# Kernel tuning notes

Hardware: AMD Instinct MI355X
Metric: run time of the kernel (lower is better)

Reference implementation:

```python
import jax, jax.numpy as jnp
import numpy as np
from jax import lax

B, C, H, W = 16, 128, 96, 96
G, S = 4, 2            # DySample groups, scale
CO = 2 * G * S * S     # offset channels = 32
COUT = 64              # EUCB2 out_channels
BN_EPS = 1e-5


def conv2d(x, w, pad=0, dil=1, groups=1):
    return lax.conv_general_dilated(
        x, w, (1, 1), [(pad, pad), (pad, pad)],
        rhs_dilation=(dil, dil), feature_group_count=groups,
        dimension_numbers=('NCHW', 'OIHW', 'NCHW'))


def init_pos():
    # torch: arange((-s+1)/2,(s-1)/2+1)/s ; meshgrid ij ; stack ; transpose(1,2) ; repeat(1,G,1)
    h = (jnp.arange(S, dtype=jnp.float32) - (S - 1) / 2) / S
    gy, gx = jnp.meshgrid(h, h, indexing='ij')
    m = jnp.stack([gy, gx])                 # [2,S,S]
    m = jnp.swapaxes(m, 1, 2)               # transpose(1,2)
    m = jnp.tile(m, (1, G, 1))              # [2, S*G, S]
    return m.reshape(1, -1, 1, 1)           # [1, 2*G*S^2, 1, 1]


def grid_sample_border(x, grid):
    # x: [N,Cg,H,W], grid: [N,Ho,Wo,2] (x,y in [-1,1]), align_corners=False, border pad
    N, Cg, Hi, Wi = x.shape
    Ho, Wo = grid.shape[1], grid.shape[2]
    ix = jnp.clip(((grid[..., 0] + 1.0) * Wi - 1.0) * 0.5, 0.0, Wi - 1.0)
    iy = jnp.clip(((grid[..., 1] + 1.0) * Hi - 1.0) * 0.5, 0.0, Hi - 1.0)
    x0f = jnp.floor(ix); y0f = jnp.floor(iy)
    wx = (ix - x0f)[:, None]                # [N,1,Ho,Wo]
    wy = (iy - y0f)[:, None]
    x0 = jnp.clip(x0f.astype(jnp.int32), 0, Wi - 1)
    x1 = jnp.clip(x0 + 1, 0, Wi - 1)
    y0 = jnp.clip(y0f.astype(jnp.int32), 0, Hi - 1)
    y1 = jnp.clip(y0 + 1, 0, Hi - 1)
    flat = x.reshape(N, Cg, Hi * Wi)

    def gather(yi, xi):
        idx = (yi * Wi + xi).reshape(N, -1)
        return jax.vmap(lambda f, i: f[:, i])(flat, idx).reshape(N, Cg, Ho, Wo)

    v00 = gather(y0, x0); v01 = gather(y0, x1)
    v10 = gather(y1, x0); v11 = gather(y1, x1)
    return (v00 * (1 - wx) * (1 - wy) + v01 * wx * (1 - wy)
            + v10 * (1 - wx) * wy + v11 * wx * wy)


def setup_inputs() -> dict:
    key = jax.random.key(0)
    ks = jax.random.split(key, 11)
    inp = {
        'x': jax.random.normal(ks[0], (B, C, H, W), jnp.float32),
        'Wo1': jax.random.normal(ks[1], (CO, C, 1, 1), jnp.float32) * 0.001,
        'bo1': jnp.zeros((CO,), jnp.float32),
        'Wo2': jax.random.normal(ks[2], (CO, CO, 3, 3), jnp.float32) * 0.001,
        'Wdw': jax.random.normal(ks[3], (C, 1, 3, 3), jnp.float32) * 0.3,
        'bn_gamma': jax.random.uniform(ks[4], (C,), jnp.float32) * 0.5 + 0.75,
        'bn_beta': jax.random.normal(ks[5], (C,), jnp.float32) * 0.1,
        'bn_mean': jax.random.normal(ks[6], (C,), jnp.float32) * 0.1,
        'bn_var': jax.random.uniform(ks[7], (C,), jnp.float32) * 0.5 + 0.5,
        'Wpw': jax.random.normal(ks[8], (COUT, C, 1, 1), jnp.float32) / np.sqrt(C),
        'bpw': jax.random.normal(ks[9], (COUT,), jnp.float32) * 0.01,
    }
    return inp


def reference(x, Wo1, bo1, Wo2, Wdw, bn_gamma, bn_beta, bn_mean, bn_var, Wpw, bpw):
    # ---- offset branch: 1x1 conv (+bias) -> 3x3 dilated(2) conv (no bias) ----
    off = conv2d(x, Wo1) + bo1[:, None, None]
    off = conv2d(off, Wo2, pad=2, dil=2)
    offset = off / G + init_pos()                    # [B, 2*G*S^2, H, W]

    # ---- DySample.sample ----
    Bc, _, Hc, Wc = offset.shape
    offset = offset.reshape(Bc, 2, G * S * S, Hc, Wc)
    ar_h = jnp.arange(Hc, dtype=jnp.float32)
    ar_w = jnp.arange(Wc, dtype=jnp.float32)
    ch = ar_h + jnp.sin(jnp.pi * (ar_h + 1.0) / Hc)
    cw = ar_w + jnp.sin(jnp.pi * (ar_w + 1.0) / Wc)
    # channel 0 -> x coord (varies with w), channel 1 -> y coord (varies with h)
    base = jnp.stack([jnp.broadcast_to(cw[None, :], (Hc, Wc)),
                      jnp.broadcast_to(ch[:, None], (Hc, Wc))])   # [2,H,W]
    norm = jnp.array([Wc, Hc], jnp.float32).reshape(1, 2, 1, 1, 1)
    coords = 2.0 * (base[None, :, None] + offset) / norm - 1.0     # [B,2,G*S^2,H,W]

    # pixel_shuffle(scale=S) on [B, 2*G*S^2, H, W]
    coords = coords.reshape(Bc, 2, G, S, S, Hc, Wc)
    coords = coords.transpose(0, 1, 2, 5, 3, 6, 4)                 # [B,2,G,H,S,W,S]
    coords = coords.reshape(Bc, 2, G, S * Hc, S * Wc)
    grid = coords.transpose(0, 2, 3, 4, 1).reshape(Bc * G, S * Hc, S * Wc, 2)

    up = grid_sample_border(x.reshape(Bc * G, C // G, Hc, Wc), grid)
    up = up.reshape(Bc, C, S * Hc, S * Wc)                         # [B,C,2H,2W]

    # ---- EUCB2: depthwise conv -> BN -> ReLU -> channel_shuffle(C) -> 1x1 conv ----
    y = conv2d(up, Wdw, pad=1, groups=C)
    y = (y - bn_mean[:, None, None]) * (bn_gamma[:, None, None]
        * lax.rsqrt(bn_var + BN_EPS)[:, None, None]) + bn_beta[:, None, None]
    y = jax.nn.relu(y)
    # channel_shuffle with groups == num_channels => channels_per_group = 1 => identity
    out = conv2d(y, Wpw) + bpw[:, None, None]
    return out
```

## Files before the change

### kernel.cpp

```cpp
#include <hip/hip_runtime.h>
#include <math.h>

typedef _Float16 f16x8 __attribute__((ext_vector_type(8)));
typedef _Float16 f16x2 __attribute__((ext_vector_type(2)));
typedef float f32x4 __attribute__((ext_vector_type(4)));

namespace {
constexpr int B_ = 16, C_ = 128, H_ = 96, W_ = 96;
constexpr int HW_ = H_ * W_;
constexpr int G_ = 4, S_ = 2;
constexpr int CO_ = 32;
constexpr int COUT_ = 64;
constexpr int HO_ = 192, WO_ = 192;
constexpr int HWO_ = HO_ * WO_;
constexpr int CPG_ = C_ / G_;
constexpr int TH_ = 8, TW_ = 32;
constexpr int HALO_H = TH_ + 2, HALO_W = TW_ + 2;
constexpr int NPOS = HALO_H * HALO_W;
constexpr int NITEM = NPOS * 4;
constexpr int TILES = (WO_ / TW_) * (HO_ / TH_);
constexpr int BPI = HW_ / 256;
constexpr int XPB = HW_ / 64;

constexpr size_t WS_XT     = 0;
constexpr size_t WS_OFF1T  = 9437184;
constexpr size_t WS_SREC   = 11796480;
constexpr size_t WS_WPWH   = 16515072;
constexpr size_t WS_WO1H   = 16519168;
constexpr size_t WS_WO2H   = 16521216;
constexpr size_t WS_WDWSH  = 16525824;
constexpr size_t WS_BIAS2H = 16526400;
constexpr size_t WS_Y      = 16526464;
constexpr size_t IMG_YF16  = (size_t)G_ * 4 * HWO_ * 8;
constexpr size_t Y_FULL_F  = (size_t)B_ * IMG_YF16 / 2;
constexpr size_t NEED_FULL = (WS_Y + Y_FULL_F) * 4;
constexpr size_t NEED_MID  = (WS_Y + Y_FULL_F / 2) * 4;

constexpr int PREP_N = 8192 + 4096 + 9216 + 1152 + 128;
}

__device__ __forceinline__ f16x8 splat8(_Float16 s) {
  return (f16x8){s, s, s, s, s, s, s, s};
}
__device__ __forceinline__ unsigned short h2u(_Float16 h) {
  union { unsigned short u; _Float16 h; } c; c.h = h; return c.u;
}
__device__ __forceinline__ _Float16 u2h(unsigned short u) {
  union { unsigned short u; _Float16 h; } c; c.u = u; return c.h;
}

__global__ __launch_bounds__(256) void k_prep(
    const float* __restrict__ Wpw, const float* __restrict__ Wo1,
    const float* __restrict__ Wo2, const float* __restrict__ Wdw,
    const float* __restrict__ bn_gamma, const float* __restrict__ bn_beta,
    const float* __restrict__ bn_mean, const float* __restrict__ bn_var,
    _Float16* __restrict__ wpwH, _Float16* __restrict__ wo1H,
    _Float16* __restrict__ wo2H, _Float16* __restrict__ wdwSh,
    _Float16* __restrict__ bias2h) {
  int i = blockIdx.x * 256 + threadIdx.x;
  if (i < 8192) {
    wpwH[i] = (_Float16)Wpw[i];
  } else if (i < 8192 + 4096) {
    int j = i - 8192;
    wo1H[j] = (_Float16)Wo1[j];
  } else if (i < 8192 + 4096 + 9216) {
    int j = i - 8192 - 4096;
    int o = j / 288, r = j % 288;
    int tap = r / 32, ci = r % 32;
    wo2H[j] = (_Float16)Wo2[o * 288 + ci * 9 + tap];
  } else if (i < 8192 + 4096 + 9216 + 1152) {
    int j = i - 8192 - 4096 - 9216;
    int c = j / 9, t = j % 9;
    float sc = bn_gamma[c] * rsqrtf(bn_var[c] + 1e-5f);
    wdwSh[t * C_ + c] = (_Float16)(Wdw[j] * sc);
  } else if (i < PREP_N) {
    int c = i - (8192 + 4096 + 9216 + 1152);
    float sc = bn_gamma[c] * rsqrtf(bn_var[c] + 1e-5f);
    bias2h[c] = (_Float16)(bn_beta[c] - bn_mean[c] * sc);
  }
}

__global__ __launch_bounds__(256, 4) void k_xpose(const float* __restrict__ x,
                                                  _Float16* __restrict__ xT) {
  __shared__ float t[64][130];
  int bid = blockIdx.x;
  int swz = (bid & 7) * (B_ * XPB / 8) + (bid >> 3);
  int b = swz / XPB, px0 = (swz % XPB) * 64;
  int tid = threadIdx.x;
  int lane = tid & 63, wv = tid >> 6;
  const float* xb = x + (size_t)b * C_ * HW_ + px0 + lane;
  for (int c = wv; c < C_; c += 4) t[lane][c] = xb[(size_t)c * HW_];
  __syncthreads();
  _Float16* ob = xT + ((size_t)b * HW_ + px0) * C_;
#pragma unroll
  for (int k = 0; k < 4; ++k) {
    int cid = tid + 256 * k;
    int px = cid >> 4, part = cid & 15;
    f16x8 v;
#pragma unroll
    for (int j = 0; j < 8; ++j) v[j] = (_Float16)t[px][part * 8 + j];
    *(f16x8*)&ob[(size_t)px * C_ + part * 8] = v;
  }
}

__global__ __launch_bounds__(256, 4) void k_off1m(
    const _Float16* __restrict__ xT, const _Float16* __restrict__ wo1H,
    const float* __restrict__ bo1, _Float16* __restrict__ off1t) {
  __shared__ float clds[32][257];
  int bid = blockIdx.x;
  int swz = (bid & 7) * (B_ * BPI / 8) + (bid >> 3);
  int b = swz / BPI, p0 = (swz % BPI) * 256;
  int tid = threadIdx.x;
  int lane = tid & 63, wv_ = tid >> 6;
  int lr = lane & 15, lk = lane >> 4;

  f32x4 acc[4][2];
#pragma unroll
  for (int mt = 0; mt < 4; ++mt)
#pragma unroll
    for (int nt = 0; nt < 2; ++nt) acc[mt][nt] = (f32x4){0.f, 0.f, 0.f, 0.f};

  const _Float16* xb = xT + ((size_t)b * HW_ + p0) * C_;
#pragma unroll
  for (int kk = 0; kk < 4; ++kk) {
    f16x8 afr[4];
#pragma unroll
    for (int mt = 0; mt < 4; ++mt)
      afr[mt] = *(const f16x8*)&xb[(size_t)((wv_ * 4 + mt) * 16 + lr) * C_ +
                                   kk * 32 + lk * 8];
#pragma unroll
    for (int nt = 0; nt < 2; ++nt) {
      f16x8 bfr = *(const f16x8*)&wo1H[(nt * 16 + lr) * C_ + kk * 32 + lk * 8];
#pragma unroll
      for (int mt = 0; mt < 4; ++mt)
        acc[mt][nt] = __builtin_amdgcn_mfma_f32_16x16x32_f16(afr[mt], bfr,
                                                             acc[mt][nt], 0, 0, 0);
    }
  }
#pragma unroll
  for (int nt = 0; nt < 2; ++nt)
#pragma unroll
    for (int mt = 0; mt < 4; ++mt)
#pragma unroll
      for (int r = 0; r < 4; ++r)
        clds[nt * 16 + lr][(wv_ * 4 + mt) * 16 + lk * 4 + r] = acc[mt][nt][r];
  __syncthreads();
  _Float16* orow = off1t + ((size_t)b * HW_ + p0 + tid) * 32;
#pragma unroll
  for (int q = 0; q < 4; ++q) {
    f16x8 v;
#pragma unroll
    for (int j = 0; j < 8; ++j)
      v[j] = (_Float16)(clds[q * 8 + j][tid] + bo1[q * 8 + j]);
    *(f16x8*)&orow[q * 8] = v;
  }
}

__global__ __launch_bounds__(256, 4) void k_coordsm(
    const _Float16* __restrict__ off1t, const _Float16* __restrict__ wo2H,
    uint2* __restrict__ srec) {
  __shared__ float clds[32][257];
  int bid = blockIdx.x;
  int swz = (bid & 7) * (B_ * BPI / 8) + (bid >> 3);
  int b = swz / BPI, p0 = (swz % BPI) * 256;
  int tid = threadIdx.x;
  int lane = tid & 63, wv_ = tid >> 6;
  int lr = lane & 15, lk = lane >> 4;

  f32x4 acc[4][2];
#pragma unroll
  for (int mt = 0; mt < 4; ++mt)
#pragma unroll
    for (int nt = 0; nt < 2; ++nt) acc[mt][nt] = (f32x4){0.f, 0.f, 0.f, 0.f};

  const _Float16* ob = off1t + (size_t)b * HW_ * 32;
  int hh[4], ww[4];
#pragma unroll
  for (int mt = 0; mt < 4; ++mt) {
    int px = p0 + (wv_ * 4 + mt) * 16 + lr;
    hh[mt] = px / W_;
    ww[mt] = px % W_;
  }
#pragma unroll
  for (int tap = 0; tap < 9; ++tap) {
    int dy2 = (tap / 3 - 1) * 2, dx2 = (tap % 3 - 1) * 2;
    f16x8 afr[4];
#pragma unroll
    for (int mt = 0; mt < 4; ++mt) {
      int h2 = hh[mt] + dy2, w2 = ww[mt] + dx2;
      f16x8 a = {};
      if ((unsigned)h2 < (unsigned)H_ && (unsigned)w2 < (unsigned)W_)
        a = *(const f16x8*)&ob[(size_t)(h2 * W_ + w2) * 32 + lk * 8];
      afr[mt] = a;
    }
#pragma unroll
    for (int nt = 0; nt < 2; ++nt) {
      f16x8 bfr = *(const f16x8*)&wo2H[(nt * 16 + lr) * 288 + tap * 32 + lk * 8];
#pragma unroll
      for (int mt = 0; mt < 4; ++mt)
        acc[mt][nt] = __builtin_amdgcn_mfma_f32_16x16x32_f16(afr[mt], bfr,
                                                             acc[mt][nt], 0, 0, 0);
    }
  }
#pragma unroll
  for (int nt = 0; nt < 2; ++nt)
#pragma unroll
    for (int mt = 0; mt < 4; ++mt)
#pragma unroll
      for (int r = 0; r < 4; ++r)
        clds[nt * 16 + lr][(wv_ * 4 + mt) * 16 + lk * 4 + r] = acc[mt][nt][r];
  __syncthreads();

  int px = p0 + tid;
  int h = px / W_, w = px % W_;
  float cwv = (float)w + sinf((float)M_PI * (float)(w + 1) / (float)W_);
  float chv = (float)h + sinf((float)M_PI * (float)(h + 1) / (float)H_);
  uint2* sb = srec + (size_t)b * G_ * HWO_;
#pragma unroll
  for (int g = 0; g < G_; ++g) {
#pragma unroll
    for (int sh = 0; sh < S_; ++sh) {
#pragma unroll
      for (int sw = 0; sw < S_; ++sw) {
        int idx = g * 4 + sh * 2 + sw;
        float offx = clds[idx][tid] * 0.25f + (sw ? 0.25f : -0.25f);
        float offy = clds[16 + idx][tid] * 0.25f + (sh ? 0.25f : -0.25f);
        float ix = fminf(fmaxf(cwv + offx - 0.5f, 0.f), (float)(W_ - 1));
        float iy = fminf(fmaxf(chv + offy - 0.5f, 0.f), (float)(H_ - 1));
        float x0f = floorf(ix), y0f = floorf(iy);
        float wx = ix - x0f, wy = iy - y0f;
        int x0 = (int)x0f, y0 = (int)y0f;
        unsigned dx = (x0 < W_ - 1) ? 1u : 0u;
        unsigned dy = (y0 < H_ - 1) ? 1u : 0u;
        unsigned base = (unsigned)(y0 * W_ + x0);
        unsigned short u00 = h2u((_Float16)((1.f - wx) * (1.f - wy)));
        unsigned short u01 = h2u((_Float16)(wx * (1.f - wy)));
        unsigned short u10 = h2u((_Float16)((1.f - wx) * wy));
        uint2 rec;
        rec.x = base | (dx << 14) | (dy << 15) | ((unsigned)u00 << 16);
        rec.y = (unsigned)u01 | ((unsigned)u10 << 16);
        sb[(size_t)g * HWO_ + (2 * h + sh) * WO_ + (2 * w + sw)] = rec;
      }
    }
  }
}

__global__ __launch_bounds__(256, 6) void k_sample(
    const _Float16* __restrict__ xT, const uint2* __restrict__ srec,
    const _Float16* __restrict__ wdwSh, const _Float16* __restrict__ bias2h,
    _Float16* __restrict__ y, int b0, int nimg) {
  __shared__ __align__(16) _Float16 up4[4 * NPOS * 8 + 832];

  int NWG = nimg * TILES;
  int bid = blockIdx.x;
  int swz = (bid & 7) * (NWG >> 3) + (bid >> 3);
  int bl = swz / TILES;
  int b = b0 + bl;
  int t = swz % TILES;
  int oh0 = (t / (WO_ / TW_)) * TH_;
  int ow0 = (t % (WO_ / TW_)) * TW_;
  int tid = threadIdx.x;
  int py = tid >> 5, px = tid & 31;
  int p_out = (oh0 + py) * WO_ + ow0 + px;

  const _Float16* xbase = xT + (size_t)b * HW_ * C_;
  for (int g = 0; g < G_; ++g) {
    __syncthreads();
    const uint2* sbase = srec + ((size_t)b * G_ + g) * HWO_;
    const _Float16* xg = xbase + g * CPG_;
#pragma unroll
    for (int r = 0; r < 6; ++r) {
      int wi = tid + r * 256;
      if (r == 5 && wi >= NITEM) continue;
      int p = wi >> 2, cq = wi & 3;
      int hy = oh0 + p / HALO_W - 1;
      int hx = ow0 + p % HALO_W - 1;
      f16x8 v = {};
      if (hy >= 0 && hy < HO_ && hx >= 0 && hx < WO_) {
        uint2 rc = sbase[(size_t)hy * WO_ + hx];
        int base = rc.x & 0x3FFFu;
        int dxC = ((rc.x >> 14) & 1u) << 7;
        int dyC = ((rc.x >> 15) & 1u) * 12288;
        _Float16 w00 = u2h((unsigned short)(rc.x >> 16));
        _Float16 w01 = u2h((unsigned short)(rc.y & 0xffffu));
        _Float16 w10 = u2h((unsigned short)(rc.y >> 16));
        float w11f = 1.f - (float)w00 - (float)w01 - (float)w10;
        const _Float16* a00p = xg + cq * 8 + (size_t)base * C_;
        f16x8 a00 = *(const f16x8*)a00p;
        f16x8 a01 = *(const f16x8*)(a00p + dxC);
        f16x8 a10 = *(const f16x8*)(a00p + dyC);
        f16x8 a11 = *(const f16x8*)(a00p + dyC + dxC);
        v = a00 * splat8(w00) + a01 * splat8(w01) + a10 * splat8(w10) +
            a11 * splat8((_Float16)w11f);
      }
      *(f16x8*)&up4[((size_t)cq * NPOS + p) * 8] = v;
    }
    __syncthreads();

#pragma unroll
    for (int q = 0; q < 4; ++q) {
      f16x8 acc = *(const f16x8*)&bias2h[g * CPG_ + q * 8];
#pragma unroll
      for (int tt = 0; tt < 9; ++tt) {
        int dy = tt / 3, dx = tt % 3;
        f16x8 pk = *(const f16x8*)
            &up4[((size_t)q * NPOS + (py + dy) * HALO_W + px + dx) * 8];
        f16x8 wv = *(const f16x8*)&wdwSh[tt * C_ + g * CPG_ + q * 8];
        acc += pk * wv;
      }
      f16x8 yv;
#pragma unroll
      for (int j = 0; j < 8; ++j)
        yv[j] = acc[j] > (_Float16)0.f ? acc[j] : (_Float16)0.f;
      *(f16x8*)&y[(((size_t)(bl * G_ + g) * 4 + q) * HWO_ + p_out) * 8] = yv;
    }
  }
}

__global__ __launch_bounds__(256, 4) void k_gemm(
    const _Float16* __restrict__ y, const _Float16* __restrict__ wpwH,
    const float* __restrict__ bpw, float* __restrict__ out, int b0, int nimg) {
  __shared__ float clds16[16][257];

  int NWG = nimg * TILES;
  int bid = blockIdx.x;
  int swz = (bid & 7) * (NWG >> 3) + (bid >> 3);
  int bl = swz / TILES;
  int b = b0 + bl;
  int p0 = (swz % TILES) * 256;
  int tid = threadIdx.x;
  int lane = tid & 63, wv_ = tid >> 6;
  int lr = lane & 15, lk = lane >> 4;

  f32x4 acc[4][4];
#pragma unroll
  for (int mt = 0; mt < 4; ++mt)
#pragma unroll
    for (int nt = 0; nt < 4; ++nt) acc[mt][nt] = (f32x4){0.f, 0.f, 0.f, 0.f};

  const _Float16* ybl = y + (size_t)bl * IMG_YF16;
#pragma unroll
  for (int kk = 0; kk < 4; ++kk) {
    f16x8 afr[4];
#pragma unroll
    for (int mt = 0; mt < 4; ++mt)
      afr[mt] = *(const f16x8*)&ybl[(((size_t)(kk * 4 + lk) * HWO_) + p0 +
                                     (wv_ * 4 + mt) * 16 + lr) * 8];
#pragma unroll
    for (int nt = 0; nt < 4; ++nt) {
      f16x8 bfr = *(const f16x8*)&wpwH[(nt * 16 + lr) * C_ + kk * CPG_ + lk * 8];
#pragma unroll
      for (int mt = 0; mt < 4; ++mt)
        acc[mt][nt] = __builtin_amdgcn_mfma_f32_16x16x32_f16(afr[mt], bfr,
                                                             acc[mt][nt], 0, 0, 0);
    }
  }
#pragma unroll
  for (int hq = 0; hq < 4; ++hq) {
    if (hq) __syncthreads();
#pragma unroll
    for (int mt = 0; mt < 4; ++mt) {
#pragma unroll
      for (int r = 0; r < 4; ++r)
        clds16[lr][(wv_ * 4 + mt) * 16 + lk * 4 + r] = acc[mt][hq][r];
    }
    __syncthreads();
#pragma unroll
    for (int i = 0; i < 16; ++i) {
      int o = hq * 16 + i;
      out[((size_t)b * COUT_ + o) * HWO_ + p0 + tid] = clds16[i][tid] + bpw[o];
    }
  }
}

extern "C" void kernel_launch(void* const* d_in, const int* in_sizes, int n_in,
                              void* d_out, int out_size, void* d_ws, size_t ws_size,
                              hipStream_t stream) {
  const float* x        = (const float*)d_in[0];
  const float* Wo1      = (const float*)d_in[1];
  const float* bo1      = (const float*)d_in[2];
  const float* Wo2      = (const float*)d_in[3];
  const float* Wdw      = (const float*)d_in[4];
  const float* bn_gamma = (const float*)d_in[5];
  const float* bn_beta  = (const float*)d_in[6];
  const float* bn_mean  = (const float*)d_in[7];
  const float* bn_var   = (const float*)d_in[8];
  const float* Wpw      = (const float*)d_in[9];
  const float* bpw      = (const float*)d_in[10];
  float* out = (float*)d_out;

  float* ws = (float*)d_ws;
  _Float16* xT     = (_Float16*)(ws + WS_XT);
  _Float16* off1t  = (_Float16*)(ws + WS_OFF1T);
  uint2* srec      = (uint2*)(ws + WS_SREC);
  _Float16* wpwH   = (_Float16*)(ws + WS_WPWH);
  _Float16* wo1H   = (_Float16*)(ws + WS_WO1H);
  _Float16* wo2H   = (_Float16*)(ws + WS_WO2H);
  _Float16* wdwSh  = (_Float16*)(ws + WS_WDWSH);
  _Float16* bias2h = (_Float16*)(ws + WS_BIAS2H);

  int chunk;
  _Float16* yb;
  if (ws_size >= NEED_FULL)      { chunk = 16; yb = (_Float16*)(ws + WS_Y); }
  else if (ws_size >= NEED_MID)  { chunk = 8;  yb = (_Float16*)(ws + WS_Y); }
  else                           { chunk = 1;  yb = (_Float16*)(ws + WS_OFF1T); }

  k_prep   <<<(PREP_N + 255) / 256, 256, 0, stream>>>(
      Wpw, Wo1, Wo2, Wdw, bn_gamma, bn_beta, bn_mean, bn_var,
      wpwH, wo1H, wo2H, wdwSh, bias2h);
  k_xpose  <<<B_ * XPB, 256, 0, stream>>>(x, xT);
  k_off1m  <<<B_ * BPI, 256, 0, stream>>>(xT, wo1H, bo1, off1t);
  k_coordsm<<<B_ * BPI, 256, 0, stream>>>(off1t, wo2H, srec);
  for (int c0 = 0; c0 < B_; c0 += chunk) {
    k_sample<<<chunk * TILES, 256, 0, stream>>>(xT, srec, wdwSh, bias2h, yb,
                                                c0, chunk);
    k_gemm  <<<chunk * TILES, 256, 0, stream>>>(yb, wpwH, bpw, out, c0, chunk);
  }
}
```

Before: 186.6 us.

## Fuse input transpose with offset 1x1 conv and make halo gather branchless

Merges the fp32-to-fp16 transpose kernel with the first offset 1x1 conv. The MFMA A-fragments are now read straight from the shared-memory tile that already holds the input, so the xT buffer is no longer re-read from global memory and one launch is removed. Separately, the sampling halo load now clamps coordinates and always issues the gather, then zeroes out-of-bounds results instead of branching. This adds some redundant loads at tile edges in exchange for fewer divergent branches.

```diff
diff --git a/kernel.cpp b/kernel.cpp
--- a/kernel.cpp
+++ b/kernel.cpp
@@ -80,17 +80,22 @@
   }
 }
 
-__global__ __launch_bounds__(256, 4) void k_xpose(const float* __restrict__ x,
-                                                  _Float16* __restrict__ xT) {
+__global__ __launch_bounds__(256, 4) void k_xoff(
+    const float* __restrict__ x, const _Float16* __restrict__ wo1H,
+    const float* __restrict__ bo1, _Float16* __restrict__ xT,
+    _Float16* __restrict__ off1t) {
   __shared__ float t[64][130];
   int bid = blockIdx.x;
   int swz = (bid & 7) * (B_ * XPB / 8) + (bid >> 3);
   int b = swz / XPB, px0 = (swz % XPB) * 64;
   int tid = threadIdx.x;
   int lane = tid & 63, wv = tid >> 6;
+  int lr = lane & 15, lk = lane >> 4;
+
   const float* xb = x + (size_t)b * C_ * HW_ + px0 + lane;
   for (int c = wv; c < C_; c += 4) t[lane][c] = xb[(size_t)c * HW_];
   __syncthreads();
+
   _Float16* ob = xT + ((size_t)b * HW_ + px0) * C_;
 #pragma unroll
   for (int k = 0; k < 4; ++k) {
@@ -101,58 +106,37 @@
     for (int j = 0; j < 8; ++j) v[j] = (_Float16)t[px][part * 8 + j];
     *(f16x8*)&ob[(size_t)px * C_ + part * 8] = v;
   }
-}
-
-__global__ __launch_bounds__(256, 4) void k_off1m(
-    const _Float16* __restrict__ xT, const _Float16* __restrict__ wo1H,
-    const float* __restrict__ bo1, _Float16* __restrict__ off1t) {
-  __shared__ float clds[32][257];
-  int bid = blockIdx.x;
-  int swz = (bid & 7) * (B_ * BPI / 8) + (bid >> 3);
-  int b = swz / BPI, p0 = (swz % BPI) * 256;
-  int tid = threadIdx.x;
-  int lane = tid & 63, wv_ = tid >> 6;
-  int lr = lane & 15, lk = lane >> 4;
-
-  f32x4 acc[4][2];
-#pragma unroll
-  for (int mt = 0; mt < 4; ++mt)
-#pragma unroll
-    for (int nt = 0; nt < 2; ++nt) acc[mt][nt] = (f32x4){0.f, 0.f, 0.f, 0.f};
-
-  const _Float16* xb = xT + ((size_t)b * HW_ + p0) * C_;
+
+  f32x4 acc[2];
+  acc[0] = (f32x4){0.f, 0.f, 0.f, 0.f};
+  acc[1] = (f32x4){0.f, 0.f, 0.f, 0.f};
 #pragma unroll
   for (int kk = 0; kk < 4; ++kk) {
-    f16x8 afr[4];
-#pragma unroll
-    for (int mt = 0; mt < 4; ++mt)
-      afr[mt] = *(const f16x8*)&xb[(size_t)((wv_ * 4 + mt) * 16 + lr) * C_ +
-                                   kk * 32 + lk * 8];
+    f16x8 afr;
+#pragma unroll
+    for (int j = 0; j < 8; ++j)
+      afr[j] = (_Float16)t[wv * 16 + lr][kk * 32 + lk * 8 + j];
 #pragma unroll
     for (int nt = 0; nt < 2; ++nt) {
       f16x8 bfr = *(const f16x8*)&wo1H[(nt * 16 + lr) * C_ + kk * 32 + lk * 8];
-#pragma unroll
-      for (int mt = 0; mt < 4; ++mt)
-        acc[mt][nt] = __builtin_amdgcn_mfma_f32_16x16x32_f16(afr[mt], bfr,
-                                                             acc[mt][nt], 0, 0, 0);
-    }
-  }
+      acc[nt] = __builtin_amdgcn_mfma_f32_16x16x32_f16(afr, bfr, acc[nt], 0, 0, 0);
+    }
+  }
+  __syncthreads();
+  float (*cl)[65] = (float(*)[65])t;
 #pragma unroll
   for (int nt = 0; nt < 2; ++nt)
 #pragma unroll
-    for (int mt = 0; mt < 4; ++mt)
-#pragma unroll
-      for (int r = 0; r < 4; ++r)
-        clds[nt * 16 + lr][(wv_ * 4 + mt) * 16 + lk * 4 + r] = acc[mt][nt][r];
+    for (int r = 0; r < 4; ++r)
+      cl[nt * 16 + lr][wv * 16 + lk * 4 + r] = acc[nt][r];
   __syncthreads();
-  _Float16* orow = off1t + ((size_t)b * HW_ + p0 + tid) * 32;
-#pragma unroll
-  for (int q = 0; q < 4; ++q) {
+  {
+    int px = tid >> 2, part = tid & 3;
     f16x8 v;
 #pragma unroll
     for (int j = 0; j < 8; ++j)
-      v[j] = (_Float16)(clds[q * 8 + j][tid] + bo1[q * 8 + j]);
-    *(f16x8*)&orow[q * 8] = v;
+      v[j] = (_Float16)(cl[part * 8 + j][px] + bo1[part * 8 + j]);
+    *(f16x8*)&off1t[((size_t)b * HW_ + px0 + px) * 32 + part * 8] = v;
   }
 }
 
@@ -275,24 +259,25 @@
       int p = wi >> 2, cq = wi & 3;
       int hy = oh0 + p / HALO_W - 1;
       int hx = ow0 + p % HALO_W - 1;
-      f16x8 v = {};
-      if (hy >= 0 && hy < HO_ && hx >= 0 && hx < WO_) {
-        uint2 rc = sbase[(size_t)hy * WO_ + hx];
-        int base = rc.x & 0x3FFFu;
-        int dxC = ((rc.x >> 14) & 1u) << 7;
-        int dyC = ((rc.x >> 15) & 1u) * 12288;
-        _Float16 w00 = u2h((unsigned short)(rc.x >> 16));
-        _Float16 w01 = u2h((unsigned short)(rc.y & 0xffffu));
-        _Float16 w10 = u2h((unsigned short)(rc.y >> 16));
-        float w11f = 1.f - (float)w00 - (float)w01 - (float)w10;
-        const _Float16* a00p = xg + cq * 8 + (size_t)base * C_;
-        f16x8 a00 = *(const f16x8*)a00p;
-        f16x8 a01 = *(const f16x8*)(a00p + dxC);
-        f16x8 a10 = *(const f16x8*)(a00p + dyC);
-        f16x8 a11 = *(const f16x8*)(a00p + dyC + dxC);
-        v = a00 * splat8(w00) + a01 * splat8(w01) + a10 * splat8(w10) +
-            a11 * splat8((_Float16)w11f);
-      }
+      bool inb = ((unsigned)hy < (unsigned)HO_) && ((unsigned)hx < (unsigned)WO_);
+      int hyc = min(max(hy, 0), HO_ - 1);
+      int hxc = min(max(hx, 0), WO_ - 1);
+      uint2 rc = sbase[(size_t)hyc * WO_ + hxc];
+      int base = rc.x & 0x3FFFu;
+      int dxC = ((rc.x >> 14) & 1u) << 7;
+      int dyC = ((rc.x >> 15) & 1u) * 12288;
+      _Float16 w00 = u2h((unsigned short)(rc.x >> 16));
+      _Float16 w01 = u2h((unsigned short)(rc.y & 0xffffu));
+      _Float16 w10 = u2h((unsigned short)(rc.y >> 16));
+      float w11f = 1.f - (float)w00 - (float)w01 - (float)w10;
+      const _Float16* a00p = xg + cq * 8 + (size_t)base * C_;
+      f16x8 a00 = *(const f16x8*)a00p;
+      f16x8 a01 = *(const f16x8*)(a00p + dxC);
+      f16x8 a10 = *(const f16x8*)(a00p + dyC);
+      f16x8 a11 = *(const f16x8*)(a00p + dyC + dxC);
+      f16x8 v = a00 * splat8(w00) + a01 * splat8(w01) + a10 * splat8(w10) +
+                a11 * splat8((_Float16)w11f);
+      if (!inb) v = (f16x8){};
       *(f16x8*)&up4[((size_t)cq * NPOS + p) * 8] = v;
     }
     __syncthreads();
@@ -408,8 +393,7 @@
   k_prep   <<<(PREP_N + 255) / 256, 256, 0, stream>>>(
       Wpw, Wo1, Wo2, Wdw, bn_gamma, bn_beta, bn_mean, bn_var,
       wpwH, wo1H, wo2H, wdwSh, bias2h);
-  k_xpose  <<<B_ * XPB, 256, 0, stream>>>(x, xT);
-  k_off1m  <<<B_ * BPI, 256, 0, stream>>>(xT, wo1H, bo1, off1t);
+  k_xoff   <<<B_ * XPB, 256, 0, stream>>>(x, wo1H, bo1, xT, off1t);
   k_coordsm<<<B_ * BPI, 256, 0, stream>>>(off1t, wo2H, srec);
   for (int c0 = 0; c0 < B_; c0 += chunk) {
     k_sample<<<chunk * TILES, 256, 0, stream>>>(xT, srec, wdwSh, bias2h, yb,
```

New measurement: 181.1 us. 1.03x faster.
